# Kernel tuning notes

Hardware: AMD Instinct MI355X
Metric: run time of the kernel (lower is better)

The kernel has to match this reference:

```python
import jax, jax.numpy as jnp
import numpy as np

B, E, S = 2, 1024, 2048
H = 16
D_QK = D_V = D_OUT = 1024
NEG = -1e4


def setup_inputs() -> dict:
    key = jax.random.key(0)
    ks = jax.random.split(key, 12)
    q = jax.random.normal(ks[0], (B, E, 1, S), jnp.float32)
    k = jax.random.normal(ks[1], (B, E, 1, S), jnp.float32)
    v = jax.random.normal(ks[2], (B, E, 1, S), jnp.float32)
    # causal qk_mask: (B, src, 1, tgt); src index > tgt index is masked
    causal = jnp.where(jnp.arange(S)[:, None] > jnp.arange(S)[None, :], NEG, 0.0).astype(jnp.float32)
    qk_mask = jnp.broadcast_to(causal[None, :, None, :], (B, S, 1, S))
    k_mask = jnp.zeros((B, S, 1, 1), jnp.float32)
    sc = 1.0 / np.sqrt(E)
    Wq = jax.random.normal(ks[3], (D_QK, E), jnp.float32) * sc
    Wk = jax.random.normal(ks[4], (D_QK, E), jnp.float32) * sc
    Wv = jax.random.normal(ks[5], (D_V, E), jnp.float32) * sc
    Wo = jax.random.normal(ks[6], (D_OUT, D_V), jnp.float32) * sc
    bq = jnp.zeros((D_QK,), jnp.float32)
    bk = jnp.zeros((D_QK,), jnp.float32)
    bv = jnp.zeros((D_V,), jnp.float32)
    bo = jnp.zeros((D_OUT,), jnp.float32)
    return {"q": q, "k": k, "v": v, "qk_mask": qk_mask, "k_mask": k_mask,
            "Wq": Wq, "bq": bq, "Wk": Wk, "bk": bk, "Wv": Wv, "bv": bv,
            "Wo": Wo, "bo": bo}


def reference(q, k, v, qk_mask, k_mask, Wq, bq, Wk, bk, Wv, bv, Wo, bo):
    b, _, _, tq = q.shape
    sk = k.shape[3]
    d_qk, d_v = Wq.shape[0], Wv.shape[0]
    dh, dvh = d_qk // H, d_v // H
    fact = float(dh) ** (-0.5)
    # 1x1 conv projections on (B, C, 1, S) == matmul over channels
    qp = jnp.einsum('oc,bcis->bois', Wq, q) + bq[None, :, None, None]
    kp = jnp.einsum('oc,bcis->bois', Wk, k) + bk[None, :, None, None]
    vp = jnp.einsum('oc,bcis->bois', Wv, v) + bv[None, :, None, None]
    # split heads: channel dim is head-major (contiguous chunks)
    qh = qp[:, :, 0, :].reshape(b, H, dh, tq)
    kh = kp[:, :, 0, :].reshape(b, H, dh, sk)
    vh = vp[:, :, 0, :].reshape(b, H, dvh, sk)
    # scores: (B, H, src, tgt); masks broadcast over heads
    scores = jnp.einsum('bhcq,bhck->bhkq', qh, kh) * fact
    scores = scores + qk_mask[:, None, :, 0, :] + k_mask[:, None, :, 0, 0][..., None]
    w = jax.nn.softmax(scores, axis=2)  # softmax over src (k) axis
    attn = jnp.einsum('bhkq,bhck->bhcq', w, vh).reshape(b, d_v, 1, tq)
    out = jnp.einsum('oc,bcis->bois', Wo, attn) + bo[None, :, None, None]
    return out
```

## Files before the change

kernel.cpp:

```cpp
#include <hip/hip_runtime.h>
#include <hip/hip_bf16.h>
#include <stdint.h>

typedef unsigned short u16;
typedef __attribute__((ext_vector_type(8))) short short8;
typedef __attribute__((ext_vector_type(4))) short short4v;
typedef __attribute__((ext_vector_type(4))) float f32x4;

#define MFMA16(a,b,c) __builtin_amdgcn_mfma_f32_16x16x32_bf16((a),(b),(c),0,0,0)
#define EXP2F(x) __builtin_amdgcn_exp2f(x)

typedef const __attribute__((address_space(1))) void glb_void;
typedef __attribute__((address_space(3))) void lds_void;

__device__ __forceinline__ u16 f2b(float f){
  unsigned u = __float_as_uint(f);
  u += 0x7fffu + ((u>>16)&1u);
  return (u16)(u>>16);
}
__device__ __forceinline__ unsigned pack_bf16(float a, float b){
  __hip_bfloat162 h = __float22bfloat162_rn(make_float2(a,b));
  unsigned u; __builtin_memcpy(&u, &h, 4); return u;
}
__device__ __forceinline__ void gld16(const void* g, void* l){
  __builtin_amdgcn_global_load_lds((glb_void*)g, (lds_void*)l, 16, 0, 0);
}

__device__ __forceinline__ void stage128x64_sw(const u16* g, u16* lds, int gstride, int w, int lane){
  const int sub = lane>>3, c16 = lane&7;
  const int gcol = (c16 ^ sub)<<3;
  #pragma unroll
  for (int i=0;i<4;++i){
    int r0 = (w*4+i)*8;
    gld16(g + (size_t)(r0 + sub)*gstride + gcol, lds + r0*64);
  }
}
__device__ __forceinline__ void stage64x64_sw(const u16* g, u16* lds, int gstride, int w, int lane){
  const int sub = lane>>3, c16 = lane&7;
  const int gcol = (c16 ^ sub)<<3;
  #pragma unroll
  for (int i=0;i<2;++i){
    int r0 = (w*2+i)*8;
    gld16(g + (size_t)(r0 + sub)*gstride + gcol, lds + r0*64);
  }
}
__device__ __forceinline__ const short8* frag64(const u16* lds, int row, int c16){
  return (const short8*)(lds + row*64 + ((c16 ^ (row&7))<<3));
}
__device__ __forceinline__ void stage64x128_sw(const u16* g, u16* lds, int gstride, int w, int lane){
  const int sub = lane>>4, c16 = lane&15;
  #pragma unroll
  for (int i=0;i<4;++i){
    int r0 = (w*4+i)*4;
    int row = r0 + sub;
    gld16(g + (size_t)row*gstride + ((c16 ^ (row&15))<<3), lds + r0*128);
  }
}
__device__ __forceinline__ const short8* frag128(const u16* lds, int row, int c16){
  return (const short8*)(lds + row*128 + ((c16 ^ (row&15))<<3));
}

__global__ __launch_bounds__(256) void prep(
    const float* __restrict__ q, const float* __restrict__ k, const float* __restrict__ v,
    const float* __restrict__ qkm, const float* __restrict__ km,
    const float* __restrict__ Wq, const float* __restrict__ Wk,
    const float* __restrict__ Wv, const float* __restrict__ Wo,
    u16* __restrict__ W16, char* __restrict__ classes,
    u16* __restrict__ qT, u16* __restrict__ kT, u16* __restrict__ vT)
{
  __shared__ __align__(16) float t[64][72];
  const int bx = blockIdx.x, tid = threadIdx.x;
  const int S = 2048, E = 1024, nW = E*E;

  if (bx < 2048){
    const int sel = bx>>9, blk = bx&511;
    const float* src = sel==0?Wq : sel==1?Wk : sel==2?Wv : Wo;
    const float sc = (sel==0) ? 0.18033688f : 1.0f;
    u16* dst = W16 + (size_t)sel*nW;
    int i = (blk*256 + tid)*8;
    float4 a = *(const float4*)(src+i);
    float4 b = *(const float4*)(src+i+4);
    short8 o;
    o[0]=(short)f2b(a.x*sc); o[1]=(short)f2b(a.y*sc); o[2]=(short)f2b(a.z*sc); o[3]=(short)f2b(a.w*sc);
    o[4]=(short)f2b(b.x*sc); o[5]=(short)f2b(b.y*sc); o[6]=(short)f2b(b.z*sc); o[7]=(short)f2b(b.w*sc);
    *(short8*)(dst+i) = o;
  } else if (bx < 4096){
    const int tt = bx - 2048;
    const int b = tt>>10, qi = (tt>>5)&31, ki = tt&31;
    const int k0 = ki*64, q0 = qi*64;
    int az = 1, an = 1;
    #pragma unroll
    for (int p=0;p<4;++p){
      int e = tid + p*256;
      int row = e>>4, c4 = (e&15)*4;
      float kmv = km[(size_t)b*S + k0 + row];
      float4 mv = *(const float4*)&qkm[((size_t)b*S + k0 + row)*S + q0 + c4];
      mv.x += kmv; mv.y += kmv; mv.z += kmv; mv.w += kmv;
      az &= (mv.x==0.f) & (mv.y==0.f) & (mv.z==0.f) & (mv.w==0.f);
      an &= (mv.x<-1e3f) & (mv.y<-1e3f) & (mv.z<-1e3f) & (mv.w<-1e3f);
    }
    const int az_all = __syncthreads_and(az);
    const int an_all = __syncthreads_and(an);
    if (tid==0)
      classes[((size_t)b*32 + qi)*32 + ki] = an_all ? 2 : (az_all ? 0 : 1);
  } else {
    const int tt = bx - 4096;
    const int tensor = tt>>10, r = tt&1023;
    const int b = r>>9, rr = r&511;
    const int c0 = (rr>>5)*64, s0 = (rr&31)*64;
    const float* x = tensor==0 ? q : tensor==1 ? k : v;
    u16* xt = tensor==0 ? qT : tensor==1 ? kT : vT;
    #pragma unroll
    for (int p=0;p<4;++p){
      int e = tid + p*256;
      int row = e>>4, c4 = (e&15)*4;
      *(float4*)&t[row][c4] = *(const float4*)&x[((size_t)b*E + c0 + row)*S + s0 + c4];
    }
    __syncthreads();
    #pragma unroll
    for (int p=0;p<2;++p){
      int e = tid + p*256;
      int row = e>>3, col8 = (e&7)*8;
      short8 o;
      #pragma unroll
      for (int u=0;u<8;++u) o[u] = (short)f2b(t[col8+u][row]);
      *(short8*)&xt[((size_t)b*S + s0 + row)*E + c0 + col8] = o;
    }
  }
}

template<bool F32OUT>
__device__ __forceinline__ void gemm_core(
    const u16* __restrict__ A, const u16* __restrict__ Bt, const float* __restrict__ bias,
    float bscale, void* __restrict__ Cv, size_t cbase, int N, int K, int bias_on_m,
    int m0, int n0, u16* As, u16* Bs)
{
  const int tid = threadIdx.x, w = tid>>6, lane = tid&63;
  const int ln = lane&15, quad = lane>>4;
  const int m0w = (w>>1)*64, n0w = (w&1)*64;
  f32x4 acc[4][4];
  #pragma unroll
  for(int i=0;i<4;++i)
    #pragma unroll
    for(int j=0;j<4;++j) acc[i][j] = f32x4{0.f,0.f,0.f,0.f};

  for (int kc=0; kc<K; kc+=64){
    __syncthreads();
    stage128x64_sw(A  + (size_t)m0*K + kc, As, K, w, lane);
    stage128x64_sw(Bt + (size_t)n0*K + kc, Bs, K, w, lane);
    __syncthreads();
    #pragma unroll
    for (int kk=0; kk<64; kk+=32){
      const int c16 = (kk>>3) + quad;
      short8 af[4], bf[4];
      #pragma unroll
      for (int mt=0;mt<4;++mt) af[mt] = *frag64(As, m0w+mt*16+ln, c16);
      #pragma unroll
      for (int nt=0;nt<4;++nt) bf[nt] = *frag64(Bs, n0w+nt*16+ln, c16);
      #pragma unroll
      for (int mt=0;mt<4;++mt)
        #pragma unroll
        for (int nt=0;nt<4;++nt)
          acc[mt][nt] = MFMA16(af[mt], bf[nt], acc[mt][nt]);
    }
  }
  #pragma unroll
  for (int mt=0;mt<4;++mt){
    #pragma unroll
    for (int nt=0;nt<4;++nt){
      const int col = n0 + n0w + nt*16 + ln;
      const float bn = bias_on_m ? 0.f : bias[col]*bscale;
      #pragma unroll
      for (int r=0;r<4;++r){
        const int row = m0 + m0w + mt*16 + quad*4 + r;
        const float bb = bias_on_m ? bias[row]*bscale : bn;
        const float val = acc[mt][nt][r] + bb;
        const size_t idx = cbase + (size_t)row*N + col;
        if (F32OUT) ((float*)Cv)[idx] = val;
        else        ((u16*)Cv)[idx]   = f2b(val);
      }
    }
  }
}

__global__ __launch_bounds__(256,3) void proj(
    const u16* __restrict__ qT, const u16* __restrict__ kT, const u16* __restrict__ vT,
    const u16* __restrict__ W16,
    const float* __restrict__ bq, const float* __restrict__ bk, const float* __restrict__ bv,
    u16* __restrict__ Qb, u16* __restrict__ Kb, u16* __restrict__ Vb)
{
  __shared__ __align__(16) u16 As[128*64];
  __shared__ __align__(16) u16 Bs[128*64];
  const int bx = blockIdx.x;
  const int zone = bx>>7, r = bx&127;
  const size_t sSE = (size_t)2048*1024;
  const int nW = 1024*1024;
  if (zone < 4){
    const int sel = zone>>1, b = zone&1;
    const int m0 = (r>>3)*128, n0 = (r&7)*128;
    gemm_core<false>((sel? kT : qT) + b*sSE, W16 + (size_t)sel*nW, sel? bk : bq,
                     sel? 1.0f : 0.18033688f, sel? Kb : Qb, b*sSE,
                     1024, 1024, 0, m0, n0, As, Bs);
  } else {
    const int b = zone&1;
    const int m0 = (r>>4)*128, n0 = (r&15)*128;
    gemm_core<false>(W16 + (size_t)2*nW, vT + b*sSE, bv,
                     1.0f, Vb, b*sSE,
                     2048, 1024, 1, m0, n0, As, Bs);
  }
}

__global__ __launch_bounds__(256,4) void gemm_out64(
    const u16* __restrict__ Wo16, const u16* __restrict__ At, const float* __restrict__ bo,
    float* __restrict__ out)
{
  __shared__ __align__(16) u16 As[64*64];
  __shared__ __align__(16) u16 Bs[128*64];
  const int b = blockIdx.z;
  const int m0 = blockIdx.y*64, n0 = blockIdx.x*128;
  const size_t sSE = (size_t)2048*1024;
  const int K = 1024, N = 2048;
  const u16* Bt = At + b*sSE;
  const int tid = threadIdx.x, w = tid>>6, lane = tid&63;
  const int ln = lane&15, quad = lane>>4;
  const int m0w = (w>>1)*32, n0w = (w&1)*64;
  f32x4 acc[2][4];
  #pragma unroll
  for(int i=0;i<2;++i)
    #pragma unroll
    for(int j=0;j<4;++j) acc[i][j] = f32x4{0.f,0.f,0.f,0.f};

  for (int kc=0; kc<K; kc+=64){
    __syncthreads();
    stage64x64_sw (Wo16 + (size_t)m0*K + kc, As, K, w, lane);
    stage128x64_sw(Bt   + (size_t)n0*K + kc, Bs, K, w, lane);
    __syncthreads();
    #pragma unroll
    for (int kk=0; kk<64; kk+=32){
      const int c16 = (kk>>3) + quad;
      short8 af[2], bf[4];
      #pragma unroll
      for (int mt=0;mt<2;++mt) af[mt] = *frag64(As, m0w+mt*16+ln, c16);
      #pragma unroll
      for (int nt=0;nt<4;++nt) bf[nt] = *frag64(Bs, n0w+nt*16+ln, c16);
      #pragma unroll
      for (int mt=0;mt<2;++mt)
        #pragma unroll
        for (int nt=0;nt<4;++nt)
          acc[mt][nt] = MFMA16(af[mt], bf[nt], acc[mt][nt]);
    }
  }
  #pragma unroll
  for (int mt=0;mt<2;++mt){
    #pragma unroll
    for (int nt=0;nt<4;++nt){
      const int col = n0 + n0w + nt*16 + ln;
      #pragma unroll
      for (int r=0;r<4;++r){
        const int row = m0 + m0w + mt*16 + quad*4 + r;
        out[b*sSE + (size_t)row*N + col] = acc[mt][nt][r] + bo[row];
      }
    }
  }
}

__global__ __launch_bounds__(256,2) void attn(
    const u16* __restrict__ Qb, const u16* __restrict__ Kb, const u16* __restrict__ Vb,
    const float* __restrict__ qk_mask, const float* __restrict__ k_mask,
    const char* __restrict__ classes, u16* __restrict__ Ot)
{
  __shared__ __align__(16) u16 Ks[128*64];
  __shared__ __align__(16) u16 Vs[64*128];
  const int x = blockIdx.x;
  const int b = x&1, h = (x>>1)&15;
  const int pp = x>>5, pair = pp>>1, half = pp&1;
  const int tid = threadIdx.x, w = tid>>6, lane = tid&63;
  const int ln = lane&15, quad = lane>>4;
  const int S = 2048;
  const float LOG2E = 1.44269504f, C2 = 16.0f;

  #pragma unroll
  for (int sub=0; sub<2; ++sub){
    const int qt = sub ? pair : (15-pair);
    const int qbase = qt*128 + half*64;
    const int qg = qbase + w*16 + ln;
    short8 qf[2];
    #pragma unroll
    for (int kkI=0;kkI<2;++kkI)
      qf[kkI] = *(const short8*)&Qb[((size_t)b*S + qg)*1024 + h*64 + kkI*32 + quad*8];

    const char* cl = classes + ((size_t)b*32 + qt*2 + half)*32;
    float rs = 0.f;
    f32x4 acc[4];
    #pragma unroll
    for (int ct=0;ct<4;++ct) acc[ct] = f32x4{0.f,0.f,0.f,0.f};

    for (int kt=0; kt<16; ++kt){
      const char c0 = cl[2*kt], c1 = cl[2*kt+1];
      if (c0==2 && c1==2) continue;
      const bool nomask = (c0|c1)==0;
      const int k0 = kt*128;
      __syncthreads();
      stage128x64_sw(Kb + ((size_t)b*S + k0)*1024 + h*64, Ks, 1024, w, lane);
      stage64x128_sw(Vb + ((size_t)b*1024 + h*64)*S + k0, Vs, S, w, lane);
      __syncthreads();

      unsigned pk[8][2];
      #pragma unroll
      for (int t=0;t<8;++t){
        f32x4 s = f32x4{0.f,0.f,0.f,0.f};
        #pragma unroll
        for (int kkI=0;kkI<2;++kkI)
          s = MFMA16(*frag64(Ks, t*16+ln, kkI*4 + quad), qf[kkI], s);
        float e[4];
        if (nomask){
          #pragma unroll
          for (int r=0;r<4;++r) e[r] = EXP2F(s[r] - C2);
        } else {
          #pragma unroll
          for (int r=0;r<4;++r){
            const int kg = k0 + t*16 + quad*4 + r;
            const float m = qk_mask[((size_t)b*S + kg)*S + qg] + k_mask[(size_t)b*S + kg];
            e[r] = EXP2F(fmaf(m, LOG2E, s[r]) - C2);
          }
        }
        rs += (e[0]+e[1]) + (e[2]+e[3]);
        pk[t][0] = pack_bf16(e[0], e[1]);
        pk[t][1] = pack_bf16(e[2], e[3]);
      }
      const int srcA = (quad&1)*32 + ln, srcB = srcA + 16;
      const bool hi = (quad>>1)&1;
      #pragma unroll
      for (int c=0;c<4;++c){
        unsigned a0 = __shfl((int)pk[2*c][0],   srcA, 64);
        unsigned a1 = __shfl((int)pk[2*c][1],   srcA, 64);
        unsigned a2 = __shfl((int)pk[2*c][0],   srcB, 64);
        unsigned a3 = __shfl((int)pk[2*c][1],   srcB, 64);
        unsigned b0 = __shfl((int)pk[2*c+1][0], srcA, 64);
        unsigned b1 = __shfl((int)pk[2*c+1][1], srcA, 64);
        unsigned b2 = __shfl((int)pk[2*c+1][0], srcB, 64);
        unsigned b3 = __shfl((int)pk[2*c+1][1], srcB, 64);
        short8 pf;
        ((unsigned*)&pf)[0] = hi ? b0 : a0;
        ((unsigned*)&pf)[1] = hi ? b1 : a1;
        ((unsigned*)&pf)[2] = hi ? b2 : a2;
        ((unsigned*)&pf)[3] = hi ? b3 : a3;
        #pragma unroll
        for (int ct=0;ct<4;++ct)
          acc[ct] = MFMA16(*frag128(Vs, ct*16+ln, c*4 + quad), pf, acc[ct]);
      }
    }
    rs += __shfl_xor(rs, 16, 64);
    rs += __shfl_xor(rs, 32, 64);
    const float rinv = 1.0f / rs;
    #pragma unroll
    for (int ct=0;ct<4;++ct){
      short4v o4;
      #pragma unroll
      for (int r=0;r<4;++r) o4[r] = (short)f2b(acc[ct][r] * rinv);
      *(short4v*)&Ot[((size_t)b*S + qg)*1024 + h*64 + ct*16 + quad*4] = o4;
    }
  }
}

extern "C" void kernel_launch(void* const* d_in, const int* in_sizes, int n_in,
                              void* d_out, int out_size, void* d_ws, size_t ws_size,
                              hipStream_t stream)
{
  const float* q   = (const float*)d_in[0];
  const float* k   = (const float*)d_in[1];
  const float* v   = (const float*)d_in[2];
  const float* qkm = (const float*)d_in[3];
  const float* km  = (const float*)d_in[4];
  const float* Wq  = (const float*)d_in[5];
  const float* bq  = (const float*)d_in[6];
  const float* Wk  = (const float*)d_in[7];
  const float* bk  = (const float*)d_in[8];
  const float* Wv  = (const float*)d_in[9];
  const float* bv  = (const float*)d_in[10];
  const float* Wo  = (const float*)d_in[11];
  const float* bo  = (const float*)d_in[12];
  float* out = (float*)d_out;

  const size_t nAct = (size_t)2*2048*1024;
  const int   nW   = 1024*1024;

  u16* A0 = (u16*)d_ws;
  u16* A1 = A0 + nAct;
  u16* A2 = A1 + nAct;
  u16* A3 = A2 + nAct;
  u16* A4 = A3 + nAct;
  u16* A5 = A4 + nAct;
  u16* W16 = A5 + nAct;
  char* classes = (char*)(W16 + (size_t)4*nW);
  u16* Wo16 = W16 + (size_t)3*nW;

  dim3 blk(256);
  prep      <<<dim3(7168), blk, 0, stream>>>(q, k, v, qkm, km, Wq, Wk, Wv, Wo,
                                             W16, classes, A0, A1, A2);
  proj      <<<dim3(768),  blk, 0, stream>>>(A0, A1, A2, W16, bq, bk, bv, A3, A4, A5);
  attn      <<<dim3(512),  blk, 0, stream>>>(A3, A4, A5, qkm, km, classes, A0);
  gemm_out64<<<dim3(16,16,2), blk, 0, stream>>>(Wo16, A0, bo, out);
}
```

Measured before the change: 254.7 us.

## Split-K output GEMM with atomics and stage two KV tiles per attention step

The output projection GEMM is split along K into two halves. Each half accumulates into a zeroed output buffer with atomicAdd, which doubles the number of blocks, and a memset is added before the kernels. Separately, the attention kernel now loads two 128-key K/V tiles per barrier pair. This halves the number of __syncthreads, but it doubles LDS use and register pressure from pk, which may reduce occupancy. The atomics add memory traffic and make the summation order nondeterministic.

```diff
diff --git a/kernel.cpp b/kernel.cpp
--- a/kernel.cpp
+++ b/kernel.cpp
@@ -216,7 +216,7 @@
 {
   __shared__ __align__(16) u16 As[64*64];
   __shared__ __align__(16) u16 Bs[128*64];
-  const int b = blockIdx.z;
+  const int zz = blockIdx.z, b = zz>>1, kh = zz&1;
   const int m0 = blockIdx.y*64, n0 = blockIdx.x*128;
   const size_t sSE = (size_t)2048*1024;
   const int K = 1024, N = 2048;
@@ -230,7 +230,7 @@
     #pragma unroll
     for(int j=0;j<4;++j) acc[i][j] = f32x4{0.f,0.f,0.f,0.f};
 
-  for (int kc=0; kc<K; kc+=64){
+  for (int kc=kh*512; kc<kh*512+512; kc+=64){
     __syncthreads();
     stage64x64_sw (Wo16 + (size_t)m0*K + kc, As, K, w, lane);
     stage128x64_sw(Bt   + (size_t)n0*K + kc, Bs, K, w, lane);
@@ -258,7 +258,8 @@
       #pragma unroll
       for (int r=0;r<4;++r){
         const int row = m0 + m0w + mt*16 + quad*4 + r;
-        out[b*sSE + (size_t)row*N + col] = acc[mt][nt][r] + bo[row];
+        const float val = acc[mt][nt][r] + (kh ? 0.f : bo[row]);
+        atomicAdd(&out[b*sSE + (size_t)row*N + col], val);
       }
     }
   }
@@ -269,8 +270,8 @@
     const float* __restrict__ qk_mask, const float* __restrict__ k_mask,
     const char* __restrict__ classes, u16* __restrict__ Ot)
 {
-  __shared__ __align__(16) u16 Ks[128*64];
-  __shared__ __align__(16) u16 Vs[64*128];
+  __shared__ __align__(16) u16 Ks[2][128*64];
+  __shared__ __align__(16) u16 Vs[2][64*128];
   const int x = blockIdx.x;
   const int b = x&1, h = (x>>1)&15;
   const int pp = x>>5, pair = pp>>1, half = pp&1;
@@ -295,59 +296,70 @@
     #pragma unroll
     for (int ct=0;ct<4;++ct) acc[ct] = f32x4{0.f,0.f,0.f,0.f};
 
-    for (int kt=0; kt<16; ++kt){
-      const char c0 = cl[2*kt], c1 = cl[2*kt+1];
-      if (c0==2 && c1==2) continue;
-      const bool nomask = (c0|c1)==0;
-      const int k0 = kt*128;
+    for (int kp=0; kp<8; ++kp){
+      const int kt0 = 2*kp;
+      const char a0=cl[2*kt0], a1=cl[2*kt0+1], b0c=cl[2*kt0+2], b1c=cl[2*kt0+3];
+      if (a0==2 && a1==2 && b0c==2 && b1c==2) continue;
+      const bool nm[2] = { (a0|a1)==0, (b0c|b1c)==0 };
       __syncthreads();
-      stage128x64_sw(Kb + ((size_t)b*S + k0)*1024 + h*64, Ks, 1024, w, lane);
-      stage64x128_sw(Vb + ((size_t)b*1024 + h*64)*S + k0, Vs, S, w, lane);
+      #pragma unroll
+      for (int tI=0;tI<2;++tI){
+        const int k0 = (kt0+tI)*128;
+        stage128x64_sw(Kb + ((size_t)b*S + k0)*1024 + h*64, Ks[tI], 1024, w, lane);
+        stage64x128_sw(Vb + ((size_t)b*1024 + h*64)*S + k0, Vs[tI], S, w, lane);
+      }
       __syncthreads();
 
-      unsigned pk[8][2];
-      #pragma unroll
-      for (int t=0;t<8;++t){
-        f32x4 s = f32x4{0.f,0.f,0.f,0.f};
+      unsigned pk[2][8][2];
+      #pragma unroll
+      for (int tI=0;tI<2;++tI){
+        const int k0 = (kt0+tI)*128;
         #pragma unroll
-        for (int kkI=0;kkI<2;++kkI)
-          s = MFMA16(*frag64(Ks, t*16+ln, kkI*4 + quad), qf[kkI], s);
-        float e[4];
-        if (nomask){
+        for (int t=0;t<8;++t){
+          f32x4 s = f32x4{0.f,0.f,0.f,0.f};
           #pragma unroll
-          for (int r=0;r<4;++r) e[r] = EXP2F(s[r] - C2);
-        } else {
-          #pragma unroll
-          for (int r=0;r<4;++r){
-            const int kg = k0 + t*16 + quad*4 + r;
-            const float m = qk_mask[((size_t)b*S + kg)*S + qg] + k_mask[(size_t)b*S + kg];
-            e[r] = EXP2F(fmaf(m, LOG2E, s[r]) - C2);
+          for (int kkI=0;kkI<2;++kkI)
+            s = MFMA16(*frag64(Ks[tI], t*16+ln, kkI*4 + quad), qf[kkI], s);
+          float e[4];
+          if (nm[tI]){
+            #pragma unroll
+            for (int r=0;r<4;++r) e[r] = EXP2F(s[r] - C2);
+          } else {
+            #pragma unroll
+            for (int r=0;r<4;++r){
+              const int kg = k0 + t*16 + quad*4 + r;
+              const float m = qk_mask[((size_t)b*S + kg)*S + qg] + k_mask[(size_t)b*S + kg];
+              e[r] = EXP2F(fmaf(m, LOG2E, s[r]) - C2);
+            }
           }
+          rs += (e[0]+e[1]) + (e[2]+e[3]);
+          pk[tI][t][0] = pack_bf16(e[0], e[1]);
+          pk[tI][t][1] = pack_bf16(e[2], e[3]);
         }
-        rs += (e[0]+e[1]) + (e[2]+e[3]);
-        pk[t][0] = pack_bf16(e[0], e[1]);
-        pk[t][1] = pack_bf16(e[2], e[3]);
       }
       const int srcA = (quad&1)*32 + ln, srcB = srcA + 16;
       const bool hi = (quad>>1)&1;
       #pragma unroll
-      for (int c=0;c<4;++c){
-        unsigned a0 = __shfl((int)pk[2*c][0],   srcA, 64);
-        unsigned a1 = __shfl((int)pk[2*c][1],   srcA, 64);
-        unsigned a2 = __shfl((int)pk[2*c][0],   srcB, 64);
-        unsigned a3 = __shfl((int)pk[2*c][1],   srcB, 64);
-        unsigned b0 = __shfl((int)pk[2*c+1][0], srcA, 64);
-        unsigned b1 = __shfl((int)pk[2*c+1][1], srcA, 64);
-        unsigned b2 = __shfl((int)pk[2*c+1][0], srcB, 64);
-        unsigned b3 = __shfl((int)pk[2*c+1][1], srcB, 64);
-        short8 pf;
-        ((unsigned*)&pf)[0] = hi ? b0 : a0;
-        ((unsigned*)&pf)[1] = hi ? b1 : a1;
-        ((unsigned*)&pf)[2] = hi ? b2 : a2;
-        ((unsigned*)&pf)[3] = hi ? b3 : a3;
+      for (int tI=0;tI<2;++tI){
         #pragma unroll
-        for (int ct=0;ct<4;++ct)
-          acc[ct] = MFMA16(*frag128(Vs, ct*16+ln, c*4 + quad), pf, acc[ct]);
+        for (int c=0;c<4;++c){
+          unsigned a0s = __shfl((int)pk[tI][2*c][0],   srcA, 64);
+          unsigned a1s = __shfl((int)pk[tI][2*c][1],   srcA, 64);
+          unsigned a2s = __shfl((int)pk[tI][2*c][0],   srcB, 64);
+          unsigned a3s = __shfl((int)pk[tI][2*c][1],   srcB, 64);
+          unsigned b0s = __shfl((int)pk[tI][2*c+1][0], srcA, 64);
+          unsigned b1s = __shfl((int)pk[tI][2*c+1][1], srcA, 64);
+          unsigned b2s = __shfl((int)pk[tI][2*c+1][0], srcB, 64);
+          unsigned b3s = __shfl((int)pk[tI][2*c+1][1], srcB, 64);
+          short8 pf;
+          ((unsigned*)&pf)[0] = hi ? b0s : a0s;
+          ((unsigned*)&pf)[1] = hi ? b1s : a1s;
+          ((unsigned*)&pf)[2] = hi ? b2s : a2s;
+          ((unsigned*)&pf)[3] = hi ? b3s : a3s;
+          #pragma unroll
+          for (int ct=0;ct<4;++ct)
+            acc[ct] = MFMA16(*frag128(Vs[tI], ct*16+ln, c*4 + quad), pf, acc[ct]);
+        }
       }
     }
     rs += __shfl_xor(rs, 16, 64);
@@ -396,9 +408,10 @@
   u16* Wo16 = W16 + (size_t)3*nW;
 
   dim3 blk(256);
+  hipMemsetAsync(out, 0, (size_t)out_size*sizeof(float), stream);
   prep      <<<dim3(7168), blk, 0, stream>>>(q, k, v, qkm, km, Wq, Wk, Wv, Wo,
                                              W16, classes, A0, A1, A2);
   proj      <<<dim3(768),  blk, 0, stream>>>(A0, A1, A2, W16, bq, bk, bv, A3, A4, A5);
   attn      <<<dim3(512),  blk, 0, stream>>>(A3, A4, A5, qkm, km, classes, A0);
-  gemm_out64<<<dim3(16,16,2), blk, 0, stream>>>(Wo16, A0, bo, out);
-}
+  gemm_out64<<<dim3(16,16,4), blk, 0, stream>>>(Wo16, A0, bo, out);
+}
```

Result: slower. 277.6 us (+9.0%).
